# Kernel tuning notes

Measured on AMD Instinct MI355X. Metric: run time of the kernel, lower is better.

Reference implementation:

```python
import jax, jax.numpy as jnp
import numpy as np

B_, L_, H_, D_, N_, R_, K_ = 2, 1024, 2048, 4096, 16, 128, 4


def setup_inputs() -> dict:
    key = jax.random.key(0)
    ks = jax.random.split(key, 8)
    s = lambda k, shp, sc: jax.random.normal(k, shp, jnp.float32) * sc
    x = s(ks[0], (B_, L_, H_), 1.0)
    in_proj_w = s(ks[1], (2 * D_, H_), 0.02)
    conv_w = s(ks[2], (D_, 1, K_), 0.1)          # depthwise conv kernel (OIW, I=1)
    conv_b = s(ks[3], (D_,), 0.02)
    x_proj_w = s(ks[4], (R_ + 2 * N_, D_), 0.02)
    dt_proj_w = s(ks[5], (D_, R_), 0.02)
    dt_proj_b = s(ks[6], (D_,), 0.02)
    # A_log init as in module: log(arange(1..N)) expanded over channels
    A_log = jnp.log(jnp.broadcast_to(jnp.arange(1, N_ + 1, dtype=jnp.float32), (D_, N_)))
    D = jnp.ones((D_,), jnp.float32)
    out_proj_w = s(ks[7], (H_, D_), 0.02)
    return dict(x=x, in_proj_w=in_proj_w, conv_w=conv_w, conv_b=conv_b,
                x_proj_w=x_proj_w, dt_proj_w=dt_proj_w, dt_proj_b=dt_proj_b,
                A_log=A_log, D=D, out_proj_w=out_proj_w)


def reference(x, in_proj_w, conv_w, conv_b, x_proj_w, dt_proj_w, dt_proj_b, A_log, D, out_proj_w):
    Bsz, L, H = x.shape
    # in_proj -> split into ssm branch and gate branch
    proj = x @ in_proj_w.T                               # [B, L, 2D]
    h, gate = jnp.split(proj, 2, axis=-1)                # each [B, L, D]
    # causal depthwise conv1d over time (left pad K-1, truncate to L)
    hc = h.transpose(0, 2, 1)                            # [B, D, L]
    conv = jax.lax.conv_general_dilated(
        hc, conv_w, window_strides=(1,), padding=[(K_ - 1, 0)],
        dimension_numbers=('NCW', 'OIW', 'NCW'), feature_group_count=hc.shape[1])
    u = jax.nn.silu(conv + conv_b[None, :, None]).transpose(0, 2, 1)  # [B, L, D]
    # input-dependent SSM parameters
    ssm_p = u @ x_proj_w.T                               # [B, L, R+2N]
    dt, Bm, Cm = jnp.split(ssm_p, [R_, R_ + N_], axis=-1)
    dt = jax.nn.softplus(dt @ dt_proj_w.T + dt_proj_b)   # [B, L, D]
    A = -jnp.exp(A_log)                                  # [D, N]

    def step(state, inp):
        dt_t, B_t, C_t, u_t = inp                        # [B,D],[B,N],[B,N],[B,D]
        dA = jnp.exp(dt_t[:, :, None] * A)               # [B, D, N]
        dBu = dt_t[:, :, None] * B_t[:, None, :] * u_t[:, :, None]
        state = state * dA + dBu                         # [B, D, N]
        y = jnp.einsum('bdn,bn->bd', state, C_t)
        return state, y

    init = jnp.zeros((Bsz, u.shape[-1], N_), x.dtype)
    _, ys = jax.lax.scan(step, init, (dt.transpose(1, 0, 2), Bm.transpose(1, 0, 2),
                                      Cm.transpose(1, 0, 2), u.transpose(1, 0, 2)))
    y = ys.transpose(1, 0, 2)                            # [B, L, D]
    y = (y + u * D) * jax.nn.silu(gate)
    return y @ out_proj_w.T                              # [B, L, H]
```

## Files before the change

### kernel.cpp

```cpp
#include <hip/hip_runtime.h>
#include <hip/hip_bf16.h>
#include <cstdint>
#include <cstddef>

typedef __hip_bfloat16 bf16;
typedef __attribute__((ext_vector_type(8))) short short8;
typedef __attribute__((ext_vector_type(4))) float f32x4;

#define BB 2
#define LL 1024
#define HH 2048
#define DD 4096
#define NN 16
#define RR 128
#define KK 4
#define TT (BB*LL)
#define NC 16
#define LC (LL/NC)
#define KSPLIT 8

__device__ __forceinline__ void gload_lds16(const void* g, void* l) {
  __builtin_amdgcn_global_load_lds(
      (__attribute__((address_space(1))) void*)(g),
      (__attribute__((address_space(3))) void*)(l), 16, 0, 0);
}

__global__ void probe_dtype(const unsigned int* __restrict__ alog, int* __restrict__ flag) {
  if (threadIdx.x == 0 && blockIdx.x == 0) *flag = (alog[0] != 0u) ? 1 : 0;
}

__global__ __launch_bounds__(256) void cvt_bf16(
    const void* __restrict__ src, bf16* __restrict__ dst,
    int n4, const int* __restrict__ flag)
{
  const bool isb = (*flag != 0);
  const int stride = gridDim.x * blockDim.x;
  for (int i = blockIdx.x * blockDim.x + threadIdx.x; i < n4; i += stride) {
    if (isb) {
      ((uint2*)dst)[i] = ((const uint2*)src)[i];
    } else {
      float4 v = ((const float4*)src)[i];
      dst[i*4+0] = __float2bfloat16(v.x);
      dst[i*4+1] = __float2bfloat16(v.y);
      dst[i*4+2] = __float2bfloat16(v.z);
      dst[i*4+3] = __float2bfloat16(v.w);
    }
  }
}

template<int EPI>
__global__ __launch_bounds__(512, 1) void gemm256(
    const bf16* __restrict__ A, const bf16* __restrict__ Bw,
    bf16* __restrict__ Cb, float* __restrict__ Cf,
    int M, int N, int K, int ldk)
{
  __shared__ __align__(16) short As[2*256*64];
  __shared__ __align__(16) short Bs[2*256*64];
  const int tid = threadIdx.x;
  const int w = tid >> 6, l = tid & 63;
  const int lr = l & 15, lk = l >> 4;
  const int wr = w >> 2, wc = w & 3;
  const int m0 = blockIdx.x * 256, n0 = blockIdx.y * 256;

  int kofs = 0, nt = K >> 6;
  if constexpr (EPI == 5) {
    const int z = blockIdx.z;
    kofs = z * 1344;
    nt = (z == 2) ? 22 : 21;
  }

  const int srow = w*8 + (l>>3);
  const int scol = (((l&7) ^ (l>>3)) << 3);
  const int sld  = srow*64 + (l&7)*8;

  f32x4 acc[8][4] = {};

  const bf16* Ab = A  + (size_t)m0 * ldk + kofs;
  const bf16* Bb = Bw + (size_t)n0 * ldk + kofs;

  auto stage = [&](int t) {
    const int buf = (t & 1) * 16384;
    const size_t kk = (size_t)(t << 6);
#pragma unroll
    for (int i = 0; i < 4; i++)
      gload_lds16(Ab + (size_t)(i*64 + srow) * ldk + kk + scol, &As[buf + i*4096 + sld]);
#pragma unroll
    for (int i = 0; i < 4; i++)
      gload_lds16(Bb + (size_t)(i*64 + srow) * ldk + kk + scol, &Bs[buf + i*4096 + sld]);
  };

  stage(0);
  stage(1);
  asm volatile("s_waitcnt vmcnt(8)" ::: "memory");
  __builtin_amdgcn_s_barrier();

  for (int t = 0; t < nt; ++t) {
    const int buf = (t & 1) * 16384;
    short8 bfr[4][2];
#pragma unroll
    for (int nf = 0; nf < 4; nf++) {
      const int r = wc*64 + nf*16 + lr;
#pragma unroll
      for (int ks = 0; ks < 2; ks++)
        bfr[nf][ks] = *(const short8*)&Bs[buf + r*64 + (((ks*4+lk) ^ (r&7)) << 3)];
    }
#pragma unroll
    for (int q = 0; q < 4; q++) {
      short8 afr[2][2];
#pragma unroll
      for (int mi = 0; mi < 2; mi++) {
        const int r = wr*128 + (q*2+mi)*16 + lr;
#pragma unroll
        for (int ks = 0; ks < 2; ks++)
          afr[mi][ks] = *(const short8*)&As[buf + r*64 + (((ks*4+lk) ^ (r&7)) << 3)];
      }
#pragma unroll
      for (int mi = 0; mi < 2; mi++)
#pragma unroll
        for (int nf = 0; nf < 4; nf++)
#pragma unroll
          for (int ks = 0; ks < 2; ks++)
            acc[q*2+mi][nf] = __builtin_amdgcn_mfma_f32_16x16x32_bf16(
                afr[mi][ks], bfr[nf][ks], acc[q*2+mi][nf], 0, 0, 0);
    }
    if (t + 1 < nt) {
      asm volatile("" ::: "memory");
      __builtin_amdgcn_s_barrier();
      if (t + 2 < nt) {
        stage(t + 2);
        asm volatile("s_waitcnt vmcnt(8)" ::: "memory");
      } else {
        asm volatile("s_waitcnt vmcnt(0)" ::: "memory");
      }
      __builtin_amdgcn_s_barrier();
    }
  }

#pragma unroll
  for (int mf = 0; mf < 8; mf++)
#pragma unroll
    for (int nf = 0; nf < 4; nf++)
#pragma unroll
      for (int r = 0; r < 4; r++) {
        const int row = m0 + wr*128 + mf*16 + lk*4 + r;
        const int col = n0 + wc*64 + nf*16 + lr;
        const float v = acc[mf][nf][r];
        if constexpr (EPI == 0) {
          Cb[(size_t)row*N + col] = __float2bfloat16(v);
        } else {
          Cf[(size_t)blockIdx.z*M*N + (size_t)row*N + col] = v;
        }
      }
}

__global__ __launch_bounds__(256) void reduce_out(
    const float* __restrict__ part, bf16* __restrict__ ob, float* __restrict__ of,
    const int* __restrict__ flag)
{
  const int id = blockIdx.x*256 + threadIdx.x;
  const bool isb = (*flag != 0);
  float4 a = ((const float4*)part)[id];
  const float4 b = ((const float4*)(part + (size_t)TT*HH))[id];
  const float4 c = ((const float4*)(part + (size_t)2*TT*HH))[id];
  a.x += b.x + c.x; a.y += b.y + c.y; a.z += b.z + c.z; a.w += b.w + c.w;
  if (isb) {
    ob[id*4+0] = __float2bfloat16(a.x);
    ob[id*4+1] = __float2bfloat16(a.y);
    ob[id*4+2] = __float2bfloat16(a.z);
    ob[id*4+3] = __float2bfloat16(a.w);
  } else {
    ((float4*)of)[id] = a;
  }
}

template<int EPI>
__global__ __launch_bounds__(256) void gemm_bt(
    const bf16* __restrict__ A, const bf16* __restrict__ Bw,
    bf16* __restrict__ Cb, float* __restrict__ Cf,
    const void* __restrict__ bias,
    int M, int N, int K, int ldk, int Nvalid, const int* __restrict__ flag)
{
  __shared__ __align__(16) short As[3*128*32];
  __shared__ __align__(16) short Bs[3*128*32];
  const int tid = threadIdx.x;
  const int w = tid >> 6, l = tid & 63;
  const int lr = l & 15, lk = l >> 4;
  const int m0 = blockIdx.x * 128, n0 = blockIdx.y * 128;
  const int wm = (w >> 1) * 64, wn = (w & 1) * 64;

  f32x4 acc[4][4] = {};

  const int sr0 = (w*2+0)*16 + (l>>2);
  const int sr1 = (w*2+1)*16 + (l>>2);
  const int sc0 = (((l&3) ^ ((sr0>>1)&3)) << 3);
  const int sc1 = (((l&3) ^ ((sr1>>1)&3)) << 3);
  const int lo0 = (w*2+0)*512 + l*8;
  const int lo1 = (w*2+1)*512 + l*8;

  const size_t arow0 = (size_t)(m0 + sr0);
  const size_t arow1 = (size_t)(m0 + sr1);
  const size_t brow0 = (size_t)min(n0 + sr0, N-1);
  const size_t brow1 = (size_t)min(n0 + sr1, N-1);
  const size_t kb = (size_t)blockIdx.z * K;

  const int NT = K >> 5;

  auto stage = [&](int t) {
    const int s = t % 3;
    const size_t ko = kb + (size_t)(t << 5);
    gload_lds16(A  + arow0*ldk + ko + sc0, &As[s*4096 + lo0]);
    gload_lds16(A  + arow1*ldk + ko + sc1, &As[s*4096 + lo1]);
    gload_lds16(Bw + brow0*ldk + ko + sc0, &Bs[s*4096 + lo0]);
    gload_lds16(Bw + brow1*ldk + ko + sc1, &Bs[s*4096 + lo1]);
  };

  stage(0);
  stage(1);
  asm volatile("s_waitcnt vmcnt(4)" ::: "memory");
  __builtin_amdgcn_s_barrier();

  for (int t = 0; t < NT; ++t) {
    if (t + 2 < NT) stage(t + 2);
    const int s = t % 3;
    short8 a[4], b[4];
#pragma unroll
    for (int m = 0; m < 4; m++) {
      const int row = wm + m*16 + lr;
      a[m] = *(const short8*)&As[s*4096 + row*32 + ((lk ^ ((row>>1)&3)) << 3)];
    }
#pragma unroll
    for (int n = 0; n < 4; n++) {
      const int row = wn + n*16 + lr;
      b[n] = *(const short8*)&Bs[s*4096 + row*32 + ((lk ^ ((row>>1)&3)) << 3)];
    }
#pragma unroll
    for (int m = 0; m < 4; m++)
#pragma unroll
      for (int n = 0; n < 4; n++)
        acc[m][n] = __builtin_amdgcn_mfma_f32_16x16x32_bf16(a[m], b[n], acc[m][n], 0, 0, 0);

    if (t + 2 < NT) {
      asm volatile("s_waitcnt vmcnt(4)" ::: "memory");
      __builtin_amdgcn_s_barrier();
    } else if (t + 1 < NT) {
      asm volatile("s_waitcnt vmcnt(0)" ::: "memory");
      __builtin_amdgcn_s_barrier();
    }
  }

  bool isb = false;
  if constexpr (EPI == 1) isb = (*flag != 0);

#pragma unroll
  for (int m = 0; m < 4; m++) {
#pragma unroll
    for (int n = 0; n < 4; n++) {
#pragma unroll
      for (int r = 0; r < 4; r++) {
        const int row = m0 + wm + m*16 + lk*4 + r;
        const int col = n0 + wn + n*16 + lr;
        float v = acc[m][n][r];
        if constexpr (EPI == 1) {
          const float bv = isb ? __bfloat162float(((const bf16*)bias)[col])
                               : ((const float*)bias)[col];
          v += bv;
          v = fmaxf(v, 0.f) + log1pf(expf(-fabsf(v)));
          Cb[(size_t)row*N + col] = __float2bfloat16(v);
        } else {
          if (col < Nvalid)
            Cf[(size_t)blockIdx.z*M*Nvalid + (size_t)row*Nvalid + col] = v;
        }
      }
    }
  }
}

__global__ __launch_bounds__(256) void reduce_ssm(
    const float* __restrict__ part, float* __restrict__ ssm,
    bf16* __restrict__ dtin)
{
  const int id = blockIdx.x*256 + threadIdx.x;
  const int row = id / 160, col = id - row*160;
  float v = 0.f;
#pragma unroll
  for (int s = 0; s < KSPLIT; s++) v += part[(size_t)s*TT*160 + id];
  ssm[id] = v;
  if (col < 128) dtin[(size_t)row*128 + col] = __float2bfloat16(v);
}

__global__ __launch_bounds__(256) void conv_silu(
    const bf16* __restrict__ proj, const void* __restrict__ cw,
    const void* __restrict__ cb, bf16* __restrict__ u,
    const int* __restrict__ flag)
{
  const int d  = blockIdx.x * 256 + threadIdx.x;
  const int t0 = blockIdx.y * 64;
  const int l0 = t0 & (LL-1);
  const bool isb = (*flag != 0);
  float w0, w1, w2, w3, bv;
  if (isb) {
    const bf16* c = (const bf16*)cw;
    w0 = __bfloat162float(c[d*KK+0]); w1 = __bfloat162float(c[d*KK+1]);
    w2 = __bfloat162float(c[d*KK+2]); w3 = __bfloat162float(c[d*KK+3]);
    bv = __bfloat162float(((const bf16*)cb)[d]);
  } else {
    const float* c = (const float*)cw;
    w0 = c[d*KK+0]; w1 = c[d*KK+1]; w2 = c[d*KK+2]; w3 = c[d*KK+3];
    bv = ((const float*)cb)[d];
  }
  float hm3 = 0.f, hm2 = 0.f, hm1 = 0.f;
  if (l0 > 0) {
    hm3 = __bfloat162float(proj[(size_t)(t0-3)*(2*DD) + d]);
    hm2 = __bfloat162float(proj[(size_t)(t0-2)*(2*DD) + d]);
    hm1 = __bfloat162float(proj[(size_t)(t0-1)*(2*DD) + d]);
  }
  for (int i = 0; i < 64; i++) {
    const int t = t0 + i;
    const float hc = __bfloat162float(proj[(size_t)t*(2*DD) + d]);
    const float a = bv + w0*hm3 + w1*hm2 + w2*hm1 + w3*hc;
    const float s = a / (1.f + __expf(-a));
    u[(size_t)t*DD + d] = __float2bfloat16(s);
    hm3 = hm2; hm2 = hm1; hm1 = hc;
  }
}

__global__ __launch_bounds__(256) void scan_pass1(
    const bf16* __restrict__ dt, const bf16* __restrict__ u,
    const float* __restrict__ ssm, const void* __restrict__ Alog,
    float* __restrict__ dtsum, float* __restrict__ Sb,
    const int* __restrict__ flag)
{
  const int d = blockIdx.x * 256 + threadIdx.x;
  const int c = blockIdx.y, b = blockIdx.z;
  const bool isb = (*flag != 0);
  float Av[NN];
#pragma unroll
  for (int n = 0; n < NN; n++) {
    const float alv = isb ? __bfloat162float(((const bf16*)Alog)[d*NN + n])
                          : ((const float*)Alog)[d*NN + n];
    Av[n] = -__expf(alv);
  }
  float st[NN];
#pragma unroll
  for (int n = 0; n < NN; n++) st[n] = 0.f;
  float dsum = 0.f;
  const size_t tok0 = (size_t)b * LL + (size_t)c * LC;

  float dtv = __bfloat162float(dt[tok0*DD + d]);
  float uv  = __bfloat162float(u [tok0*DD + d]);
  float4 Bp0 = *(const float4*)&ssm[tok0*160 + RR];
  float4 Bp1 = *(const float4*)&ssm[tok0*160 + RR + 4];
  float4 Bp2 = *(const float4*)&ssm[tok0*160 + RR + 8];
  float4 Bp3 = *(const float4*)&ssm[tok0*160 + RR + 12];

  for (int i = 0; i < LC; i++) {
    const float dtc = dtv, uc = uv;
    const float Bv[NN] = {Bp0.x,Bp0.y,Bp0.z,Bp0.w, Bp1.x,Bp1.y,Bp1.z,Bp1.w,
                          Bp2.x,Bp2.y,Bp2.z,Bp2.w, Bp3.x,Bp3.y,Bp3.z,Bp3.w};
    if (i < LC-1) {
      const size_t tk = tok0 + i + 1;
      dtv = __bfloat162float(dt[tk*DD + d]);
      uv  = __bfloat162float(u [tk*DD + d]);
      Bp0 = *(const float4*)&ssm[tk*160 + RR];
      Bp1 = *(const float4*)&ssm[tk*160 + RR + 4];
      Bp2 = *(const float4*)&ssm[tk*160 + RR + 8];
      Bp3 = *(const float4*)&ssm[tk*160 + RR + 12];
    }
    const float dtu = dtc * uc;
    dsum += dtc;
#pragma unroll
    for (int n = 0; n < NN; n++) {
      const float dA = __expf(dtc * Av[n]);
      st[n] = fmaf(st[n], dA, Bv[n] * dtu);
    }
  }
  dtsum[((size_t)b*NC + c)*DD + d] = dsum;
  float4* Sp = (float4*)&Sb[(((size_t)b*NC + c)*DD + d)*NN];
  Sp[0] = make_float4(st[0],  st[1],  st[2],  st[3]);
  Sp[1] = make_float4(st[4],  st[5],  st[6],  st[7]);
  Sp[2] = make_float4(st[8],  st[9],  st[10], st[11]);
  Sp[3] = make_float4(st[12], st[13], st[14], st[15]);
}

__global__ __launch_bounds__(256) void scan_pass2(
    const float* __restrict__ dtsum, float* __restrict__ Sb,
    const void* __restrict__ Alog, const int* __restrict__ flag)
{
  const int id = blockIdx.x * 256 + threadIdx.x;
  const int b = id >> 16;
  const int r = id & (DD*NN - 1);
  const int d = r >> 4, n = r & 15;
  const bool isb = (*flag != 0);
  const float alv = isb ? __bfloat162float(((const bf16*)Alog)[d*NN + n])
                        : ((const float*)Alog)[d*NN + n];
  const float Av = -__expf(alv);
  float carry = 0.f;
  size_t sidx = (size_t)b * NC * DD * NN + r;
  size_t didx = (size_t)b * NC * DD + d;
#pragma unroll
  for (int c = 0; c < NC; c++) {
    const float p = __expf(Av * dtsum[didx]);
    const float s = Sb[sidx];
    Sb[sidx] = carry;
    carry = p * carry + s;
    sidx += (size_t)DD * NN;
    didx += (size_t)DD;
  }
}

__global__ __launch_bounds__(256) void scan_pass3(
    const bf16* __restrict__ dt, const bf16* __restrict__ u,
    const float* __restrict__ ssm, const bf16* __restrict__ proj,
    const void* __restrict__ Alog, const void* __restrict__ Dp,
    const float* __restrict__ Sb,
    bf16* __restrict__ yout, const int* __restrict__ flag)
{
  const int d = blockIdx.x * 256 + threadIdx.x;
  const int c = blockIdx.y, b = blockIdx.z;
  const bool isb = (*flag != 0);
  float Av[NN];
#pragma unroll
  for (int n = 0; n < NN; n++) {
    const float alv = isb ? __bfloat162float(((const bf16*)Alog)[d*NN + n])
                          : ((const float*)Alog)[d*NN + n];
    Av[n] = -__expf(alv);
  }
  const float Dval = isb ? __bfloat162float(((const bf16*)Dp)[d])
                         : ((const float*)Dp)[d];
  float st[NN];
  {
    const float4* Sp = (const float4*)&Sb[(((size_t)b*NC + c)*DD + d)*NN];
    float4 s0 = Sp[0], s1 = Sp[1], s2 = Sp[2], s3 = Sp[3];
    st[0]=s0.x; st[1]=s0.y; st[2]=s0.z; st[3]=s0.w;
    st[4]=s1.x; st[5]=s1.y; st[6]=s1.z; st[7]=s1.w;
    st[8]=s2.x; st[9]=s2.y; st[10]=s2.z; st[11]=s2.w;
    st[12]=s3.x; st[13]=s3.y; st[14]=s3.z; st[15]=s3.w;
  }
  const size_t tok0 = (size_t)b * LL + (size_t)c * LC;

  float dtv = __bfloat162float(dt[tok0*DD + d]);
  float uv  = __bfloat162float(u [tok0*DD + d]);
  float gv  = __bfloat162float(proj[tok0*(2*DD) + DD + d]);
  float4 Bp0 = *(const float4*)&ssm[tok0*160 + RR];
  float4 Bp1 = *(const float4*)&ssm[tok0*160 + RR + 4];
  float4 Bp2 = *(const float4*)&ssm[tok0*160 + RR + 8];
  float4 Bp3 = *(const float4*)&ssm[tok0*160 + RR + 12];
  float4 Cp0 = *(const float4*)&ssm[tok0*160 + RR + NN];
  float4 Cp1 = *(const float4*)&ssm[tok0*160 + RR + NN + 4];
  float4 Cp2 = *(const float4*)&ssm[tok0*160 + RR + NN + 8];
  float4 Cp3 = *(const float4*)&ssm[tok0*160 + RR + NN + 12];

  for (int i = 0; i < LC; i++) {
    const float dtc = dtv, uc = uv, gc = gv;
    const float Bv[NN] = {Bp0.x,Bp0.y,Bp0.z,Bp0.w, Bp1.x,Bp1.y,Bp1.z,Bp1.w,
                          Bp2.x,Bp2.y,Bp2.z,Bp2.w, Bp3.x,Bp3.y,Bp3.z,Bp3.w};
    const float Cv[NN] = {Cp0.x,Cp0.y,Cp0.z,Cp0.w, Cp1.x,Cp1.y,Cp1.z,Cp1.w,
                          Cp2.x,Cp2.y,Cp2.z,Cp2.w, Cp3.x,Cp3.y,Cp3.z,Cp3.w};
    if (i < LC-1) {
      const size_t tk = tok0 + i + 1;
      dtv = __bfloat162float(dt[tk*DD + d]);
      uv  = __bfloat162float(u [tk*DD + d]);
      gv  = __bfloat162float(proj[tk*(2*DD) + DD + d]);
      Bp0 = *(const float4*)&ssm[tk*160 + RR];
      Bp1 = *(const float4*)&ssm[tk*160 + RR + 4];
      Bp2 = *(const float4*)&ssm[tk*160 + RR + 8];
      Bp3 = *(const float4*)&ssm[tk*160 + RR + 12];
      Cp0 = *(const float4*)&ssm[tk*160 + RR + NN];
      Cp1 = *(const float4*)&ssm[tk*160 + RR + NN + 4];
      Cp2 = *(const float4*)&ssm[tk*160 + RR + NN + 8];
      Cp3 = *(const float4*)&ssm[tk*160 + RR + NN + 12];
    }
    const float dtu = dtc * uc;
    float y = uc * Dval;
#pragma unroll
    for (int n = 0; n < NN; n++) {
      const float dA = __expf(dtc * Av[n]);
      st[n] = fmaf(st[n], dA, Bv[n] * dtu);
      y = fmaf(st[n], Cv[n], y);
    }
    const float sg = gc / (1.f + __expf(-gc));
    yout[(tok0 + i)*DD + d] = __float2bfloat16(y * sg);
  }
}

extern "C" void kernel_launch(void* const* d_in, const int* in_sizes, int n_in,
                              void* d_out, int out_size, void* d_ws, size_t ws_size,
                              hipStream_t stream)
{
  const void* x    = d_in[0];
  const void* wIn  = d_in[1];
  const void* cw   = d_in[2];
  const void* cb   = d_in[3];
  const void* xw   = d_in[4];
  const void* dtw  = d_in[5];
  const void* dtb  = d_in[6];
  const void* Alog = d_in[7];
  const void* Dp   = d_in[8];
  const void* ow   = d_in[9];

  char* ws = (char*)d_ws;
  bf16*  proj  = (bf16*) (ws + 0);
  bf16*  u     = (bf16*) (ws + 33554432);
  float* ssm   = (float*)(ws + 50331648);
  bf16*  dtin  = (bf16*) (ws + 51642368);
  bf16*  dtbuf = (bf16*) (ws + 52166656);
  bf16*  yfin  = (bf16*) (ws + 68943872);
  bf16*  xb    = (bf16*) (ws + 52166656);
  bf16*  wInb  = (bf16*) (ws + 60555264);
  float* part  = (float*)(ws + 52166656);
  bf16*  owb   = (bf16*) (ws + 52166656);
  float* part6 = (float*)(ws + 0);
  float* dtsum = (float*)(ws + 51642368);
  float* Sbuf  = (float*)(ws + 85721088);
  bf16*  xwb   = (bf16*) (ws + 94109696);
  bf16*  dtwb  = (bf16*) (ws + 95420416);
  int*   flag  = (int*)  (ws + 96468992);

  probe_dtype<<<1, 64, 0, stream>>>((const unsigned int*)Alog, flag);
  cvt_bf16<<<1024, 256, 0, stream>>>(x,   xb,   (BB*LL*HH)/4,   flag);
  cvt_bf16<<<1024, 256, 0, stream>>>(wIn, wInb, (2*DD*HH)/4,    flag);
  cvt_bf16<<<256,  256, 0, stream>>>(xw,  xwb,  ((RR+2*NN)*DD)/4, flag);
  cvt_bf16<<<256,  256, 0, stream>>>(dtw, dtwb, (DD*RR)/4,      flag);

  gemm256<0><<<dim3(TT/256, (2*DD)/256), 512, 0, stream>>>(
      xb, wInb, proj, nullptr, TT, 2*DD, HH, HH);
  conv_silu<<<dim3(DD/256, TT/64), 256, 0, stream>>>(proj, cw, cb, u, flag);
  gemm_bt<4><<<dim3(TT/128, 2, KSPLIT), 256, 0, stream>>>(
      u, xwb, nullptr, part, nullptr, TT, RR + 2*NN, DD/KSPLIT, DD, RR + 2*NN, flag);
  reduce_ssm<<<dim3(TT*160/256), 256, 0, stream>>>(part, ssm, dtin);
  gemm_bt<1><<<dim3(TT/128, DD/128), 256, 0, stream>>>(
      dtin, dtwb, dtbuf, nullptr, dtb, TT, DD, RR, RR, DD, flag);
  scan_pass1<<<dim3(DD/256, NC, BB), 256, 0, stream>>>(
      dtbuf, u, ssm, Alog, dtsum, Sbuf, flag);
  scan_pass2<<<dim3(BB*DD*NN/256), 256, 0, stream>>>(dtsum, Sbuf, Alog, flag);
  scan_pass3<<<dim3(DD/256, NC, BB), 256, 0, stream>>>(
      dtbuf, u, ssm, proj, Alog, Dp, Sbuf, yfin, flag);
  cvt_bf16<<<1024, 256, 0, stream>>>(ow, owb, (HH*DD)/4, flag);
  gemm256<5><<<dim3(TT/256, HH/256, 3), 512, 0, stream>>>(
      yfin, owb, nullptr, part6, TT, HH, 0, DD);
  reduce_out<<<dim3(TT*HH/4/256), 256, 0, stream>>>(
      part6, (bf16*)d_out, (float*)d_out, flag);
}
```

Before: 321.4 us.

## Interleave B-tile prefetch into MFMA sub-steps and raise wave priority during MFMAs

The GEMM main loop no longer issues all next-tile global-to-LDS loads in one block between two barriers. B loads for tile t+2 are now spread across the q sub-iterations, after the B fragments are in registers, and A loads follow after the last sub-step. Each sub-step also gets a barrier and an s_setprio bump around its MFMA burst. The aim is to overlap memory issue with matrix math and cut the exposed stall at the end of each iteration. The cost is more barriers per K-step, which could add synchronisation overhead.

```diff
diff --git a/kernel.cpp b/kernel.cpp
--- a/kernel.cpp
+++ b/kernel.cpp
@@ -78,34 +78,43 @@
   const bf16* Ab = A  + (size_t)m0 * ldk + kofs;
   const bf16* Bb = Bw + (size_t)n0 * ldk + kofs;
 
-  auto stage = [&](int t) {
-    const int buf = (t & 1) * 16384;
-    const size_t kk = (size_t)(t << 6);
-#pragma unroll
-    for (int i = 0; i < 4; i++)
-      gload_lds16(Ab + (size_t)(i*64 + srow) * ldk + kk + scol, &As[buf + i*4096 + sld]);
-#pragma unroll
-    for (int i = 0; i < 4; i++)
-      gload_lds16(Bb + (size_t)(i*64 + srow) * ldk + kk + scol, &Bs[buf + i*4096 + sld]);
+  auto stA = [&](int t, int i) {
+    gload_lds16(Ab + (size_t)(i*64 + srow)*ldk + (size_t)(t << 6) + scol,
+                &As[(t&1)*16384 + i*4096 + sld]);
   };
-
-  stage(0);
-  stage(1);
+  auto stB = [&](int t, int i) {
+    gload_lds16(Bb + (size_t)(i*64 + srow)*ldk + (size_t)(t << 6) + scol,
+                &Bs[(t&1)*16384 + i*4096 + sld]);
+  };
+
+#pragma unroll
+  for (int i = 0; i < 4; i++) stB(0, i);
+#pragma unroll
+  for (int i = 0; i < 4; i++) stA(0, i);
+#pragma unroll
+  for (int i = 0; i < 4; i++) stB(1, i);
+#pragma unroll
+  for (int i = 0; i < 4; i++) stA(1, i);
   asm volatile("s_waitcnt vmcnt(8)" ::: "memory");
   __builtin_amdgcn_s_barrier();
 
   for (int t = 0; t < nt; ++t) {
     const int buf = (t & 1) * 16384;
+    const bool pf = (t + 2 < nt);
     short8 bfr[4][2];
 #pragma unroll
-    for (int nf = 0; nf < 4; nf++) {
-      const int r = wc*64 + nf*16 + lr;
-#pragma unroll
-      for (int ks = 0; ks < 2; ks++)
-        bfr[nf][ks] = *(const short8*)&Bs[buf + r*64 + (((ks*4+lk) ^ (r&7)) << 3)];
-    }
-#pragma unroll
     for (int q = 0; q < 4; q++) {
+      if (q == 0) {
+#pragma unroll
+        for (int nf = 0; nf < 4; nf++) {
+          const int r = wc*64 + nf*16 + lr;
+#pragma unroll
+          for (int ks = 0; ks < 2; ks++)
+            bfr[nf][ks] = *(const short8*)&Bs[buf + r*64 + (((ks*4+lk) ^ (r&7)) << 3)];
+        }
+      }
+      if (q == 1 && pf) { stB(t+2, 0); stB(t+2, 1); }
+      if (q == 2 && pf) { stB(t+2, 2); stB(t+2, 3); }
       short8 afr[2][2];
 #pragma unroll
       for (int mi = 0; mi < 2; mi++) {
@@ -114,6 +123,7 @@
         for (int ks = 0; ks < 2; ks++)
           afr[mi][ks] = *(const short8*)&As[buf + r*64 + (((ks*4+lk) ^ (r&7)) << 3)];
       }
+      __builtin_amdgcn_s_setprio(1);
 #pragma unroll
       for (int mi = 0; mi < 2; mi++)
 #pragma unroll
@@ -122,18 +132,16 @@
           for (int ks = 0; ks < 2; ks++)
             acc[q*2+mi][nf] = __builtin_amdgcn_mfma_f32_16x16x32_bf16(
                 afr[mi][ks], bfr[nf][ks], acc[q*2+mi][nf], 0, 0, 0);
-    }
-    if (t + 1 < nt) {
-      asm volatile("" ::: "memory");
+      __builtin_amdgcn_s_setprio(0);
       __builtin_amdgcn_s_barrier();
-      if (t + 2 < nt) {
-        stage(t + 2);
-        asm volatile("s_waitcnt vmcnt(8)" ::: "memory");
-      } else {
-        asm volatile("s_waitcnt vmcnt(0)" ::: "memory");
-      }
-      __builtin_amdgcn_s_barrier();
-    }
+    }
+    if (pf) {
+      stA(t+2, 0); stA(t+2, 1); stA(t+2, 2); stA(t+2, 3);
+      asm volatile("s_waitcnt vmcnt(8)" ::: "memory");
+    } else if (t + 1 < nt) {
+      asm volatile("s_waitcnt vmcnt(0)" ::: "memory");
+    }
+    __builtin_amdgcn_s_barrier();
   }
 
 #pragma unroll
```

New measurement: 341.3 us. 1.06x slower.

## Stage B/C in LDS and prefetch dt/u/gate eight tokens ahead in scan passes

Applied to the files above, without the earlier changes.

In scan_pass1 and scan_pass3 the per-chunk B (and C) vectors, which every thread in a block shares, are now loaded cooperatively into shared memory once instead of being fetched per thread from global memory on each step. The per-channel dt, u and gate loads are software-pipelined in groups of eight tokens so more loads are in flight while the recurrence runs. This raises register and LDS use per thread, which may lower occupancy, in exchange for fewer redundant global loads and better latency hiding.

```diff
diff --git a/kernel.cpp b/kernel.cpp
--- a/kernel.cpp
+++ b/kernel.cpp
@@ -333,6 +333,8 @@
   const int d = blockIdx.x * 256 + threadIdx.x;
   const int c = blockIdx.y, b = blockIdx.z;
   const bool isb = (*flag != 0);
+  const size_t tok0 = (size_t)b * LL + (size_t)c * LC;
+
   float Av[NN];
 #pragma unroll
   for (int n = 0; n < NN; n++) {
@@ -340,38 +342,48 @@
                           : ((const float*)Alog)[d*NN + n];
     Av[n] = -__expf(alv);
   }
+
+  __shared__ float Bsh[LC][NN];
+  for (int k = threadIdx.x; k < LC*4; k += 256) {
+    const int tok = k >> 2, q = k & 3;
+    *(float4*)&Bsh[tok][q*4] = *(const float4*)&ssm[(tok0 + tok)*160 + RR + q*4];
+  }
+  __syncthreads();
+
   float st[NN];
 #pragma unroll
   for (int n = 0; n < NN; n++) st[n] = 0.f;
   float dsum = 0.f;
-  const size_t tok0 = (size_t)b * LL + (size_t)c * LC;
-
-  float dtv = __bfloat162float(dt[tok0*DD + d]);
-  float uv  = __bfloat162float(u [tok0*DD + d]);
-  float4 Bp0 = *(const float4*)&ssm[tok0*160 + RR];
-  float4 Bp1 = *(const float4*)&ssm[tok0*160 + RR + 4];
-  float4 Bp2 = *(const float4*)&ssm[tok0*160 + RR + 8];
-  float4 Bp3 = *(const float4*)&ssm[tok0*160 + RR + 12];
-
-  for (int i = 0; i < LC; i++) {
-    const float dtc = dtv, uc = uv;
-    const float Bv[NN] = {Bp0.x,Bp0.y,Bp0.z,Bp0.w, Bp1.x,Bp1.y,Bp1.z,Bp1.w,
-                          Bp2.x,Bp2.y,Bp2.z,Bp2.w, Bp3.x,Bp3.y,Bp3.z,Bp3.w};
-    if (i < LC-1) {
-      const size_t tk = tok0 + i + 1;
-      dtv = __bfloat162float(dt[tk*DD + d]);
-      uv  = __bfloat162float(u [tk*DD + d]);
-      Bp0 = *(const float4*)&ssm[tk*160 + RR];
-      Bp1 = *(const float4*)&ssm[tk*160 + RR + 4];
-      Bp2 = *(const float4*)&ssm[tk*160 + RR + 8];
-      Bp3 = *(const float4*)&ssm[tk*160 + RR + 12];
-    }
-    const float dtu = dtc * uc;
-    dsum += dtc;
-#pragma unroll
-    for (int n = 0; n < NN; n++) {
-      const float dA = __expf(dtc * Av[n]);
-      st[n] = fmaf(st[n], dA, Bv[n] * dtu);
+
+  float ndt[8], nu[8];
+#pragma unroll
+  for (int j = 0; j < 8; j++) {
+    ndt[j] = __bfloat162float(dt[(tok0 + j)*DD + d]);
+    nu[j]  = __bfloat162float(u [(tok0 + j)*DD + d]);
+  }
+  for (int g = 0; g < LC/8; ++g) {
+    float cdt[8], cu[8];
+#pragma unroll
+    for (int j = 0; j < 8; j++) { cdt[j] = ndt[j]; cu[j] = nu[j]; }
+    if (g < LC/8 - 1) {
+      const size_t tb = tok0 + (size_t)(g+1)*8;
+#pragma unroll
+      for (int j = 0; j < 8; j++) {
+        ndt[j] = __bfloat162float(dt[(tb + j)*DD + d]);
+        nu[j]  = __bfloat162float(u [(tb + j)*DD + d]);
+      }
+    }
+#pragma unroll
+    for (int j = 0; j < 8; j++) {
+      const float dtc = cdt[j];
+      const float dtu = dtc * cu[j];
+      dsum += dtc;
+      const int row = g*8 + j;
+#pragma unroll
+      for (int n = 0; n < NN; n++) {
+        const float dA = __expf(dtc * Av[n]);
+        st[n] = fmaf(st[n], dA, Bsh[row][n] * dtu);
+      }
     }
   }
   dtsum[((size_t)b*NC + c)*DD + d] = dsum;
@@ -418,6 +430,8 @@
   const int d = blockIdx.x * 256 + threadIdx.x;
   const int c = blockIdx.y, b = blockIdx.z;
   const bool isb = (*flag != 0);
+  const size_t tok0 = (size_t)b * LL + (size_t)c * LC;
+
   float Av[NN];
 #pragma unroll
   for (int n = 0; n < NN; n++) {
@@ -427,6 +441,13 @@
   }
   const float Dval = isb ? __bfloat162float(((const bf16*)Dp)[d])
                          : ((const float*)Dp)[d];
+
+  __shared__ float BCsh[LC][2*NN];
+  for (int k = threadIdx.x; k < LC*8; k += 256) {
+    const int tok = k >> 3, q = k & 7;
+    *(float4*)&BCsh[tok][q*4] = *(const float4*)&ssm[(tok0 + tok)*160 + RR + q*4];
+  }
+
   float st[NN];
   {
     const float4* Sp = (const float4*)&Sb[(((size_t)b*NC + c)*DD + d)*NN];
@@ -436,50 +457,43 @@
     st[8]=s2.x; st[9]=s2.y; st[10]=s2.z; st[11]=s2.w;
     st[12]=s3.x; st[13]=s3.y; st[14]=s3.z; st[15]=s3.w;
   }
-  const size_t tok0 = (size_t)b * LL + (size_t)c * LC;
-
-  float dtv = __bfloat162float(dt[tok0*DD + d]);
-  float uv  = __bfloat162float(u [tok0*DD + d]);
-  float gv  = __bfloat162float(proj[tok0*(2*DD) + DD + d]);
-  float4 Bp0 = *(const float4*)&ssm[tok0*160 + RR];
-  float4 Bp1 = *(const float4*)&ssm[tok0*160 + RR + 4];
-  float4 Bp2 = *(const float4*)&ssm[tok0*160 + RR + 8];
-  float4 Bp3 = *(const float4*)&ssm[tok0*160 + RR + 12];
-  float4 Cp0 = *(const float4*)&ssm[tok0*160 + RR + NN];
-  float4 Cp1 = *(const float4*)&ssm[tok0*160 + RR + NN + 4];
-  float4 Cp2 = *(const float4*)&ssm[tok0*160 + RR + NN + 8];
-  float4 Cp3 = *(const float4*)&ssm[tok0*160 + RR + NN + 12];
-
-  for (int i = 0; i < LC; i++) {
-    const float dtc = dtv, uc = uv, gc = gv;
-    const float Bv[NN] = {Bp0.x,Bp0.y,Bp0.z,Bp0.w, Bp1.x,Bp1.y,Bp1.z,Bp1.w,
-                          Bp2.x,Bp2.y,Bp2.z,Bp2.w, Bp3.x,Bp3.y,Bp3.z,Bp3.w};
-    const float Cv[NN] = {Cp0.x,Cp0.y,Cp0.z,Cp0.w, Cp1.x,Cp1.y,Cp1.z,Cp1.w,
-                          Cp2.x,Cp2.y,Cp2.z,Cp2.w, Cp3.x,Cp3.y,Cp3.z,Cp3.w};
-    if (i < LC-1) {
-      const size_t tk = tok0 + i + 1;
-      dtv = __bfloat162float(dt[tk*DD + d]);
-      uv  = __bfloat162float(u [tk*DD + d]);
-      gv  = __bfloat162float(proj[tk*(2*DD) + DD + d]);
-      Bp0 = *(const float4*)&ssm[tk*160 + RR];
-      Bp1 = *(const float4*)&ssm[tk*160 + RR + 4];
-      Bp2 = *(const float4*)&ssm[tk*160 + RR + 8];
-      Bp3 = *(const float4*)&ssm[tk*160 + RR + 12];
-      Cp0 = *(const float4*)&ssm[tk*160 + RR + NN];
-      Cp1 = *(const float4*)&ssm[tk*160 + RR + NN + 4];
-      Cp2 = *(const float4*)&ssm[tk*160 + RR + NN + 8];
-      Cp3 = *(const float4*)&ssm[tk*160 + RR + NN + 12];
-    }
-    const float dtu = dtc * uc;
-    float y = uc * Dval;
-#pragma unroll
-    for (int n = 0; n < NN; n++) {
-      const float dA = __expf(dtc * Av[n]);
-      st[n] = fmaf(st[n], dA, Bv[n] * dtu);
-      y = fmaf(st[n], Cv[n], y);
-    }
-    const float sg = gc / (1.f + __expf(-gc));
-    yout[(tok0 + i)*DD + d] = __float2bfloat16(y * sg);
+  __syncthreads();
+
+  float ndt[8], nu[8], ng[8];
+#pragma unroll
+  for (int j = 0; j < 8; j++) {
+    ndt[j] = __bfloat162float(dt[(tok0 + j)*DD + d]);
+    nu[j]  = __bfloat162float(u [(tok0 + j)*DD + d]);
+    ng[j]  = __bfloat162float(proj[(tok0 + j)*(2*DD) + DD + d]);
+  }
+  for (int g = 0; g < LC/8; ++g) {
+    float cdt[8], cu[8], cg[8];
+#pragma unroll
+    for (int j = 0; j < 8; j++) { cdt[j] = ndt[j]; cu[j] = nu[j]; cg[j] = ng[j]; }
+    if (g < LC/8 - 1) {
+      const size_t tb = tok0 + (size_t)(g+1)*8;
+#pragma unroll
+      for (int j = 0; j < 8; j++) {
+        ndt[j] = __bfloat162float(dt[(tb + j)*DD + d]);
+        nu[j]  = __bfloat162float(u [(tb + j)*DD + d]);
+        ng[j]  = __bfloat162float(proj[(tb + j)*(2*DD) + DD + d]);
+      }
+    }
+#pragma unroll
+    for (int j = 0; j < 8; j++) {
+      const float dtc = cdt[j], uc = cu[j], gc = cg[j];
+      const float dtu = dtc * uc;
+      const int row = g*8 + j;
+      float y = uc * Dval;
+#pragma unroll
+      for (int n = 0; n < NN; n++) {
+        const float dA = __expf(dtc * Av[n]);
+        st[n] = fmaf(st[n], dA, BCsh[row][n] * dtu);
+        y = fmaf(st[n], BCsh[row][NN + n], y);
+      }
+      const float sg = gc / (1.f + __expf(-gc));
+      yout[(tok0 + row)*DD + d] = __float2bfloat16(y * sg);
+    }
   }
 }
 
```

Result: slower. 364.9 us (+13.5%).
